# Kernel optimization log

Measured on AMD Instinct MI355X. Metric: run time of the kernel, lower is better.

Reference implementation:

```python
import jax, jax.numpy as jnp
import numpy as np

WIN = 12     # SAMv3 window_size
HEADS = 8    # num_heads

def _window(t, win=WIN):
    B, H, W, C = t.shape
    t = t.reshape(B, H // win, win, W // win, win, C).transpose(0, 1, 3, 2, 4, 5)
    return t.reshape(B, (H // win) * (W // win), win * win, C)

def _unwindow(t, H, W, win=WIN):
    B, nW, S, C = t.shape
    t = t.reshape(B, H // win, W // win, win, win, C).transpose(0, 1, 3, 2, 4, 5)
    return t.reshape(B, H, W, C)

def _sam(fq, fkv, bias, wq, wk, wv, wo, bo):
    # Windowed, masked cross-frame multi-head attention (SAMv3).
    # fq, fkv: (B, C, H, W); bias: (B, nW, 1, 1, S) additive mask bias.
    B, C, H, W = fq.shape
    hd = C // HEADS
    scale = hd ** -0.5
    q = _window(jnp.einsum('bchw,cd->bhwd', fq, wq))   # (B,nW,S,C)
    k = _window(jnp.einsum('bchw,cd->bhwd', fkv, wk))
    v = _window(jnp.einsum('bchw,cd->bhwd', fkv, wv))
    nW, S = q.shape[1], q.shape[2]
    q = q.reshape(B, nW, S, HEADS, hd)
    k = k.reshape(B, nW, S, HEADS, hd)
    v = v.reshape(B, nW, S, HEADS, hd)
    attn = jnp.einsum('bnqhd,bnkhd->bnhqk', q, k) * scale + bias
    attn = jax.nn.softmax(attn, axis=-1)
    out = jnp.einsum('bnhqk,bnkhd->bnqhd', attn, v).reshape(B, nW, S, C)
    out = out @ wo + bo
    return _unwindow(out, H, W).transpose(0, 3, 1, 2)  # (B, C, H, W)

def setup_inputs() -> dict:
    key = jax.random.key(0)
    B, C, T, H, W = 2, 384, 2, 192, 192
    ks = jax.random.split(key, 16)
    d = {}
    d['x'] = jax.random.normal(ks[0], (B, C, T, H, W), jnp.float32)
    d['mask'] = jax.random.randint(ks[1], (B, T, 1, H, W), 0, 2, jnp.int32)
    names = ['sam1_wq', 'sam1_wk', 'sam1_wv', 'sam1_wo',
             'sam2_wq', 'sam2_wk', 'sam2_wv', 'sam2_wo',
             'proj1_w', 'proj2_w']
    for i, n in enumerate(names):
        d[n] = jax.random.normal(ks[2 + i], (C, C), jnp.float32) * 0.02
    d['sam1_bo'] = jnp.zeros((C,), jnp.float32)
    d['sam2_bo'] = jnp.zeros((C,), jnp.float32)
    d['proj1_b'] = jnp.zeros((C,), jnp.float32)
    d['proj2_b'] = jnp.zeros((C,), jnp.float32)
    return d

def reference(x, mask, sam1_wq, sam1_wk, sam1_wv, sam1_wo, sam1_bo,
              sam2_wq, sam2_wk, sam2_wv, sam2_wo, sam2_bo,
              proj1_w, proj1_b, proj2_w, proj2_b):
    # x: (B, C, T=2, H, W); mask: (B, T, 1, H, W)
    f1 = x[:, :, 0]
    f2 = x[:, :, 1]
    m = mask[:, 1, 0][..., None]                      # (B, H, W, 1), frame-2 mask
    mw = _window(m)[..., 0]                           # (B, nW, S)
    bias = jnp.where(mw == 0, -1e9, 0.0).astype(x.dtype)[:, :, None, None, :]
    o1 = _sam(f1, f2, bias, sam1_wq, sam1_wk, sam1_wv, sam1_wo, sam1_bo)
    x1 = jnp.einsum('bchw,dc->bdhw', o1, proj1_w) + proj1_b[None, :, None, None]
    o2 = _sam(f2, f1, bias, sam2_wq, sam2_wk, sam2_wv, sam2_wo, sam2_bo)
    x2 = jnp.einsum('bchw,dc->bdhw', o2, proj2_w) + proj2_b[None, :, None, None]
    return jnp.concatenate([x1[:, :, None], x2[:, :, None]], axis=2)  # (B, C, 2, H, W)
```

## Files before the change

kernel.cpp:

```cpp
#include <hip/hip_runtime.h>
#include <stdint.h>

typedef __attribute__((ext_vector_type(8))) short bf16x8;
typedef __attribute__((ext_vector_type(4))) float f32x4;

#define HW    36864
#define CCH   384
#define NPIX  73728
#define W2    147456

__device__ __forceinline__ unsigned short f2bf(float f) {
  unsigned u = __builtin_bit_cast(unsigned, f);
  u += 0x7FFFu + ((u >> 16) & 1u);
  return (unsigned short)(u >> 16);
}

typedef const unsigned int __attribute__((address_space(1)))* gas1_t;
typedef unsigned int __attribute__((address_space(3)))* las3_t;
__device__ __forceinline__ void gload16(const void* g, void* l) {
  __builtin_amdgcn_global_load_lds((gas1_t)g, (las3_t)l, 16, 0, 0);
}


__global__ void k_wt(const float* __restrict__ w0, const float* __restrict__ w1,
                     const float* __restrict__ w2, const float* __restrict__ w3,
                     const float* __restrict__ w4, const float* __restrict__ w5,
                     unsigned short* __restrict__ wt) {
  int idx = blockIdx.x * 256 + threadIdx.x;
  int w = blockIdx.y;
  const float* W;
  switch (w) { case 0: W = w0; break; case 1: W = w1; break;
               case 2: W = w2; break; case 3: W = w3; break;
               case 4: W = w4; break; default: W = w5; break; }
  const int slotmap[6] = {0, 4, 5, 3, 1, 2};
  int slot = slotmap[w];
  int c = idx / 384, d = idx % 384;
  wt[(size_t)slot * W2 + (size_t)d * 384 + c] = f2bf(W[(size_t)c * 384 + d]);
}

__global__ void k_wf(const float* __restrict__ wo1, const float* __restrict__ pj1,
                     const float* __restrict__ wo2, const float* __restrict__ pj2,
                     unsigned short* __restrict__ wfT) {
  int idx = blockIdx.x * 256 + threadIdx.x;
  int s = blockIdx.y;
  const float* wo = s ? wo2 : wo1;
  const float* pj = s ? pj2 : pj1;
  int d = idx / 384, e = idx % 384;
  float acc = 0.f;
  for (int c = 0; c < 384; ++c) acc += pj[d * 384 + c] * wo[e * 384 + c];
  wfT[(size_t)s * W2 + (size_t)d * 384 + e] = f2bf(acc);
}

__global__ void k_bf(const float* __restrict__ bo1, const float* __restrict__ pj1,
                     const float* __restrict__ pb1, const float* __restrict__ bo2,
                     const float* __restrict__ pj2, const float* __restrict__ pb2,
                     float* __restrict__ bfused) {
  int t = threadIdx.x;
  int s = t / 384, d = t % 384;
  const float* bo = s ? bo2 : bo1;
  const float* pj = s ? pj2 : pj1;
  const float* pb = s ? pb2 : pb1;
  float acc = pb[d];
  for (int c = 0; c < 384; ++c) acc += pj[d * 384 + c] * bo[c];
  bfused[t] = acc;
}

__global__ __launch_bounds__(256) void k_tx(const float* __restrict__ x,
                                            unsigned short* __restrict__ xbf) {
  __shared__ float tile[64][65];
  int p0 = blockIdx.x * 64;
  int c0 = blockIdx.y * 64;
  int bt = blockIdx.z;
  int b = bt >> 1, t = bt & 1;
  int tid = threadIdx.x;
  int cl = tid >> 2;
  int pq = (tid & 3) * 4;
  const float* src = x + (((size_t)b * CCH + (c0 + cl)) * 2 + t) * HW + p0;
#pragma unroll
  for (int i = 0; i < 4; ++i) {
    int p_l = pq + i * 16;
    float4 v = *reinterpret_cast<const float4*>(src + p_l);
    tile[cl][p_l + 0] = v.x; tile[cl][p_l + 1] = v.y;
    tile[cl][p_l + 2] = v.z; tile[cl][p_l + 3] = v.w;
  }
  __syncthreads();
  int pl = tid >> 2;
  int cq = (tid & 3) * 16;
  unsigned short* dst = xbf + ((size_t)(t * 2 + b) * HW + p0 + pl) * CCH + c0 + cq;
  bf16x8 o0, o1;
#pragma unroll
  for (int j = 0; j < 8; ++j) o0[j] = (short)f2bf(tile[cq + j][pl]);
#pragma unroll
  for (int j = 0; j < 8; ++j) o1[j] = (short)f2bf(tile[cq + 8 + j][pl]);
  *reinterpret_cast<bf16x8*>(dst) = o0;
  *reinterpret_cast<bf16x8*>(dst + 8) = o1;
}

template <int EPI>
__global__ __launch_bounds__(256) void gemm_bt(
    const unsigned short* __restrict__ A,
    const unsigned short* __restrict__ Bt,
    unsigned short* __restrict__ Cq,
    unsigned short* __restrict__ Ckv,
    int nsplit,
    float* __restrict__ Cf,
    const float* __restrict__ bias,
    int tsel, float oscale) {
  __shared__ __align__(16) unsigned short Ash[2][4096];
  __shared__ __align__(16) unsigned short Bsh[2][4096];
  const int tid = threadIdx.x;
  const int lane = tid & 63;
  const int wid = tid >> 6, wr = wid >> 1, wc = wid & 1;

  const int gx = gridDim.x;
  const int nwg = gx * gridDim.y;
  const int bid = blockIdx.x + blockIdx.y * gx;
  const int chunk = nwg >> 3;
  const int l = (bid & 7) * chunk + (bid >> 3);
  const int bx = l % gx, by = l / gx;

  const int m0 = (EPI == 1 ? bx : by) * 128;
  const int n0 = (EPI == 1 ? by : bx) * 128;
  const int r15 = lane & 15, g = lane >> 4;

  const int u1 = tid + 256;
  const unsigned short* srcA0 = A + (size_t)(m0 + (tid >> 2)) * 384 + (((tid & 3) ^ ((tid >> 3) & 3)) << 3);
  const unsigned short* srcA1 = A + (size_t)(m0 + (u1 >> 2)) * 384 + (((u1 & 3) ^ ((u1 >> 3) & 3)) << 3);
  const unsigned short* srcB0 = Bt + (size_t)(n0 + (tid >> 2)) * 384 + (((tid & 3) ^ ((tid >> 3) & 3)) << 3);
  const unsigned short* srcB1 = Bt + (size_t)(n0 + (u1 >> 2)) * 384 + (((u1 & 3) ^ ((u1 >> 3) & 3)) << 3);
  const int wbase = (tid & ~63) * 8;

  f32x4 acc[4][4];
  f32x4 zero4 = {0.f, 0.f, 0.f, 0.f};
#pragma unroll
  for (int a = 0; a < 4; ++a)
#pragma unroll
    for (int b = 0; b < 4; ++b) acc[a][b] = zero4;

  const int swzr = (g ^ ((r15 >> 1) & 3)) << 3;

#define STAGE(cur, kt) do {                            \
    int ke = (kt) * 32;                                \
    gload16(srcA0 + ke, &Ash[(cur)][wbase]);           \
    gload16(srcA1 + ke, &Ash[(cur)][2048 + wbase]);    \
    gload16(srcB0 + ke, &Bsh[(cur)][wbase]);           \
    gload16(srcB1 + ke, &Bsh[(cur)][2048 + wbase]);    \
  } while (0)

  STAGE(0, 0);
  for (int kt = 0; kt < 12; ++kt) {
    const int cur = kt & 1;
    __syncthreads();
    if (kt < 11) STAGE(cur ^ 1, kt + 1);
    bf16x8 af[4], bfv[4];
#pragma unroll
    for (int a = 0; a < 4; ++a)
      af[a] = *(const bf16x8*)&Ash[cur][(wr * 64 + a * 16 + r15) * 32 + swzr];
#pragma unroll
    for (int b = 0; b < 4; ++b)
      bfv[b] = *(const bf16x8*)&Bsh[cur][(wc * 64 + b * 16 + r15) * 32 + swzr];
#pragma unroll
    for (int a = 0; a < 4; ++a)
#pragma unroll
      for (int b = 0; b < 4; ++b)
        acc[a][b] = __builtin_amdgcn_mfma_f32_16x16x32_bf16(af[a], bfv[b], acc[a][b], 0, 0, 0);
  }
#undef STAGE

  if (EPI == 2) {
    const int bb = m0 / HW;
    unsigned short* Cp;
    int ldc, nc0;
    float sc;
    if (n0 < nsplit) { Cp = Cq;  ldc = 384; nc0 = n0;          sc = oscale; }
    else             { Cp = Ckv; ldc = 768; nc0 = n0 - nsplit; sc = 1.0f;   }
#pragma unroll
    for (int a = 0; a < 4; ++a) {
#pragma unroll
      for (int r = 0; r < 4; ++r) {
        int m = m0 + wr * 64 + a * 16 + g * 4 + r;
        int p = m - bb * HW;
        int ph = p / 192, pw = p % 192;
        int wy = ph / 12, sy = ph % 12, wx = pw / 12, sx = pw % 12;
        size_t rowoff = ((size_t)bb * HW + (wy * 16 + wx) * 144 + sy * 12 + sx) * (size_t)ldc;
#pragma unroll
        for (int b = 0; b < 4; ++b) {
          int n = nc0 + wc * 64 + b * 16 + r15;
          Cp[rowoff + n] = f2bf(acc[a][b][r] * sc);
        }
      }
    }
  } else {
    int bb = n0 / HW;
#pragma unroll
    for (int a = 0; a < 4; ++a) {
      int d = m0 + wr * 64 + a * 16 + g * 4;
#pragma unroll
      for (int b = 0; b < 4; ++b) {
        int n = n0 + wc * 64 + b * 16 + r15;
        int p = n - bb * HW;
#pragma unroll
        for (int r = 0; r < 4; ++r) {
          float v = acc[a][b][r] + bias[d + r];
          Cf[(((size_t)bb * CCH + (d + r)) * 2 + tsel) * HW + p] = v;
        }
      }
    }
  }
}

__global__ __launch_bounds__(512, 2) void attn_kernel(
    const unsigned short* __restrict__ q,
    const unsigned short* __restrict__ kv,
    const int* __restrict__ mask,
    unsigned short* __restrict__ obuf) {
  __shared__ __align__(16) unsigned short P[8][16][168];
  const int n = blockIdx.x, b = blockIdx.y;
  const int tid = threadIdx.x;
  const int h = tid >> 6, lane = tid & 63;
  const int c15 = lane & 15, g = lane >> 4;
  const int wy = n >> 4, wx = n & 15;
  const unsigned short* qb = q  + ((size_t)b * HW + n * 144) * 384 + h * 48;
  const unsigned short* kb = kv + ((size_t)b * HW + n * 144) * 768 + h * 48;
  const unsigned short* vb = kb + 384;
  const int* mrow = mask + (size_t)(b * 2 + 1) * HW;

  for (int idx = lane; idx < 16 * 24; idx += 64)
    P[h][idx / 24][144 + (idx % 24)] = 0;

  float biasv[9];
#pragma unroll
  for (int nt = 0; nt < 9; ++nt) {
    int sk = nt * 16 + c15;
    int ph = wy * 12 + sk / 12, pw = wx * 12 + sk % 12;
    biasv[nt] = (mrow[ph * 192 + pw] == 0) ? -1e9f : 0.0f;
  }

  bf16x8 zfrag = {0, 0, 0, 0, 0, 0, 0, 0};
  f32x4 zero4 = {0.f, 0.f, 0.f, 0.f};

  bf16x8 kf0[9], kf1[9];
#pragma unroll
  for (int nt = 0; nt < 9; ++nt) {
    const unsigned short* kp = kb + (size_t)(nt * 16 + c15) * 768;
    kf0[nt] = *(const bf16x8*)(kp + g * 8);
    kf1[nt] = zfrag;
    if (g < 2) kf1[nt] = *(const bf16x8*)(kp + 32 + g * 8);
  }

  bf16x8 vf[5][3];
#pragma unroll
  for (int ks = 0; ks < 5; ++ks) {
#pragma unroll
    for (int dt = 0; dt < 3; ++dt) {
      bf16x8 v = {0, 0, 0, 0, 0, 0, 0, 0};
#pragma unroll
      for (int j = 0; j < 8; ++j) {
        int sk = ks * 32 + g * 8 + j;
        if (sk < 144)
          v[j] = (short)vb[(size_t)sk * 768 + dt * 16 + c15];
      }
      vf[ks][dt] = v;
    }
  }

  bf16x8 qf0, qf1;
  {
    const unsigned short* qp = qb + (size_t)c15 * 384;
    qf0 = *(const bf16x8*)(qp + g * 8);
    qf1 = zfrag;
    if (g < 2) qf1 = *(const bf16x8*)(qp + 32 + g * 8);
  }

  for (int mt = 0; mt < 9; ++mt) {
    bf16x8 qn0 = zfrag, qn1 = zfrag;
    if (mt < 8) {
      const unsigned short* qp = qb + (size_t)((mt + 1) * 16 + c15) * 384;
      qn0 = *(const bf16x8*)(qp + g * 8);
      if (g < 2) qn1 = *(const bf16x8*)(qp + 32 + g * 8);
    }

    float l4[4] = {0.f, 0.f, 0.f, 0.f};
    f32x4 oacc[3];
#pragma unroll
    for (int dt = 0; dt < 3; ++dt) oacc[dt] = zero4;

#pragma unroll
    for (int nt = 0; nt < 9; ++nt) {
      f32x4 s = __builtin_amdgcn_mfma_f32_16x16x32_bf16(qf1, kf1[nt], zero4, 0, 0, 0);
      s = __builtin_amdgcn_mfma_f32_16x16x32_bf16(qf0, kf0[nt], s, 0, 0, 0);
#pragma unroll
      for (int r = 0; r < 4; ++r) {
        float pv = __expf(s[r] + biasv[nt]);
        l4[r] += pv;
        P[h][g * 4 + r][nt * 16 + c15] = f2bf(pv);
      }
      if (nt & 1) {
        int ks = nt >> 1;
        bf16x8 pf = *(const bf16x8*)&P[h][c15][ks * 32 + g * 8];
#pragma unroll
        for (int dt = 0; dt < 3; ++dt)
          oacc[dt] = __builtin_amdgcn_mfma_f32_16x16x32_bf16(pf, vf[ks][dt], oacc[dt], 0, 0, 0);
      }
    }
    {
      bf16x8 pf = *(const bf16x8*)&P[h][c15][4 * 32 + g * 8];
#pragma unroll
      for (int dt = 0; dt < 3; ++dt)
        oacc[dt] = __builtin_amdgcn_mfma_f32_16x16x32_bf16(pf, vf[4][dt], oacc[dt], 0, 0, 0);
    }

#pragma unroll
    for (int s = 1; s < 16; s <<= 1)
#pragma unroll
      for (int r = 0; r < 4; ++r) l4[r] += __shfl_xor(l4[r], s, 64);

    float inv[4];
#pragma unroll
    for (int r = 0; r < 4; ++r) inv[r] = 1.0f / l4[r];
#pragma unroll
    for (int dt = 0; dt < 3; ++dt) {
#pragma unroll
      for (int r = 0; r < 4; ++r) {
        int so = mt * 16 + g * 4 + r;
        int oh = wy * 12 + so / 12, ow = wx * 12 + so % 12;
        obuf[((size_t)b * HW + oh * 192 + ow) * 384 + h * 48 + dt * 16 + c15] =
            f2bf(oacc[dt][r] * inv[r]);
      }
    }

    qf0 = qn0; qf1 = qn1;
  }
}

extern "C" void kernel_launch(void* const* d_in, const int* in_sizes, int n_in,
                              void* d_out, int out_size, void* d_ws, size_t ws_size,
                              hipStream_t stream) {
  const float* x    = (const float*)d_in[0];
  const int*   mask = (const int*)d_in[1];
  const float* wq1 = (const float*)d_in[2];
  const float* wk1 = (const float*)d_in[3];
  const float* wv1 = (const float*)d_in[4];
  const float* wo1 = (const float*)d_in[5];
  const float* wq2 = (const float*)d_in[6];
  const float* wk2 = (const float*)d_in[7];
  const float* wv2 = (const float*)d_in[8];
  const float* wo2 = (const float*)d_in[9];
  const float* pj1 = (const float*)d_in[10];
  const float* pj2 = (const float*)d_in[11];
  const float* bo1 = (const float*)d_in[12];
  const float* bo2 = (const float*)d_in[13];
  const float* pb1 = (const float*)d_in[14];
  const float* pb2 = (const float*)d_in[15];
  float* out = (float*)d_out;

  const float SCALE = 0.14433756729740643f;

  char* ws = (char*)d_ws;
  size_t off = 0;
  unsigned short* wt   = (unsigned short*)(ws + off); off += (size_t)6 * W2 * 2;
  unsigned short* wfT  = (unsigned short*)(ws + off); off += (size_t)2 * W2 * 2;
  float*          bfu  = (float*)(ws + off);          off += (size_t)2 * 384 * 4;
  unsigned short* xbf  = (unsigned short*)(ws + off); off += (size_t)4 * HW * CCH * 2;
  size_t fixed = off;

  size_t qsz = (size_t)NPIX * 384 * 2, kvsz = (size_t)NPIX * 768 * 2, osz = qsz;
  bool fused = (ws_size >= fixed + 2 * qsz + 2 * kvsz + osz);
  if (!fused && ws_size < fixed + qsz + kvsz + osz) return;

  k_wt<<<dim3(576, 6), 256, 0, stream>>>(wq1, wk1, wv1, wq2, wk2, wv2, wt);
  k_wf<<<dim3(576, 2), 256, 0, stream>>>(wo1, pj1, wo2, pj2, wfT);
  k_bf<<<1, 768, 0, stream>>>(bo1, pj1, pb1, bo2, pj2, pb2, bfu);
  k_tx<<<dim3(576, 6, 4), 256, 0, stream>>>(x, xbf);

  if (fused) {
    unsigned short* qb[2] = {(unsigned short*)(ws + fixed),
                             (unsigned short*)(ws + fixed + qsz)};
    unsigned short* kvb[2] = {(unsigned short*)(ws + fixed + 2 * qsz),
                              (unsigned short*)(ws + fixed + 2 * qsz + kvsz)};
    unsigned short* obuf = (unsigned short*)(ws + fixed + 2 * qsz + 2 * kvsz);
    for (int f = 0; f < 2; ++f) {
      gemm_bt<2><<<dim3(9, 576), 256, 0, stream>>>(
          xbf + (size_t)f * 2 * HW * CCH, wt + (size_t)f * 3 * W2,
          qb[f], kvb[1 - f], 384, nullptr, nullptr, 0, SCALE);
    }
    for (int s = 0; s < 2; ++s) {
      attn_kernel<<<dim3(256, 2), 512, 0, stream>>>(qb[s], kvb[s], mask, obuf);
      gemm_bt<1><<<dim3(3, 576), 256, 0, stream>>>(
          wfT + (size_t)s * W2, obuf, nullptr, nullptr, 0, out, bfu + s * 384, s, 1.0f);
    }
  } else {
    unsigned short* qbuf = (unsigned short*)(ws + fixed);
    unsigned short* kvbuf = (unsigned short*)(ws + fixed + qsz);
    unsigned short* obuf = (unsigned short*)(ws + fixed + qsz + kvsz);
    for (int s = 0; s < 2; ++s) {
      const unsigned short* fq = xbf + (size_t)(s == 0 ? 0 : 1) * 2 * HW * CCH;
      const unsigned short* fk = xbf + (size_t)(s == 0 ? 1 : 0) * 2 * HW * CCH;
      gemm_bt<2><<<dim3(3, 576), 256, 0, stream>>>(
          fq, wt + (size_t)(s == 0 ? 0 : 3) * W2, qbuf, nullptr, 384,
          nullptr, nullptr, 0, SCALE);
      gemm_bt<2><<<dim3(6, 576), 256, 0, stream>>>(
          fk, wt + (size_t)(s == 0 ? 4 : 1) * W2, nullptr, kvbuf, 0,
          nullptr, nullptr, 0, 1.0f);
      attn_kernel<<<dim3(256, 2), 512, 0, stream>>>(qbuf, kvbuf, mask, obuf);
      gemm_bt<1><<<dim3(3, 576), 256, 0, stream>>>(
          wfT + (size_t)s * W2, obuf, nullptr, nullptr, 0, out, bfu + s * 384, s, 1.0f);
    }
  }
}
```

Before: 723.6 us.

## Triple-buffer GEMM K-loop and move window gather into attention via pixel table

The GEMM mainloop moves from double to triple buffering in one combined LDS array. Prefetch now runs two stages ahead, and each step waits on a partial vmcnt plus a raw barrier instead of a full __syncthreads. The QKV GEMM epilogue no longer scatters rows into windowed order and writes plain row-major output. The attention kernel instead builds an LDS table of pixel offsets per window and gathers Q/K/V rows and scatters outputs through it. This aims to overlap global loads with MFMA and to cut the per-element index arithmetic in the epilogue, at the cost of more LDS per GEMM block and strided gathered loads in attention.

```diff
diff --git a/kernel.cpp b/kernel.cpp
--- a/kernel.cpp
+++ b/kernel.cpp
@@ -106,8 +106,7 @@
     float* __restrict__ Cf,
     const float* __restrict__ bias,
     int tsel, float oscale) {
-  __shared__ __align__(16) unsigned short Ash[2][4096];
-  __shared__ __align__(16) unsigned short Bsh[2][4096];
+  __shared__ __align__(16) unsigned short Lsh[3][8192];
   const int tid = threadIdx.x;
   const int lane = tid & 63;
   const int wid = tid >> 6, wr = wid >> 1, wc = wid & 1;
@@ -139,55 +138,59 @@
 
   const int swzr = (g ^ ((r15 >> 1) & 3)) << 3;
 
-#define STAGE(cur, kt) do {                            \
-    int ke = (kt) * 32;                                \
-    gload16(srcA0 + ke, &Ash[(cur)][wbase]);           \
-    gload16(srcA1 + ke, &Ash[(cur)][2048 + wbase]);    \
-    gload16(srcB0 + ke, &Bsh[(cur)][wbase]);           \
-    gload16(srcB1 + ke, &Bsh[(cur)][2048 + wbase]);    \
+#define STAGE(buf, kt) do {                                  \
+    int ke = (kt) * 32;                                      \
+    gload16(srcA0 + ke, &Lsh[(buf)][wbase]);                 \
+    gload16(srcA1 + ke, &Lsh[(buf)][2048 + wbase]);          \
+    gload16(srcB0 + ke, &Lsh[(buf)][4096 + wbase]);          \
+    gload16(srcB1 + ke, &Lsh[(buf)][6144 + wbase]);          \
   } while (0)
 
+#define COMPUTE(buf) do {                                                       \
+    bf16x8 af[4], bfv[4];                                                       \
+    _Pragma("unroll")                                                           \
+    for (int a = 0; a < 4; ++a)                                                 \
+      af[a] = *(const bf16x8*)&Lsh[(buf)][(wr * 64 + a * 16 + r15) * 32 + swzr];\
+    _Pragma("unroll")                                                           \
+    for (int b = 0; b < 4; ++b)                                                 \
+      bfv[b] = *(const bf16x8*)&Lsh[(buf)][4096 + (wc * 64 + b * 16 + r15) * 32 + swzr];\
+    _Pragma("unroll")                                                           \
+    for (int a = 0; a < 4; ++a)                                                 \
+      _Pragma("unroll")                                                         \
+      for (int b = 0; b < 4; ++b)                                               \
+        acc[a][b] = __builtin_amdgcn_mfma_f32_16x16x32_bf16(af[a], bfv[b], acc[a][b], 0, 0, 0);\
+  } while (0)
+
   STAGE(0, 0);
-  for (int kt = 0; kt < 12; ++kt) {
-    const int cur = kt & 1;
-    __syncthreads();
-    if (kt < 11) STAGE(cur ^ 1, kt + 1);
-    bf16x8 af[4], bfv[4];
-#pragma unroll
-    for (int a = 0; a < 4; ++a)
-      af[a] = *(const bf16x8*)&Ash[cur][(wr * 64 + a * 16 + r15) * 32 + swzr];
-#pragma unroll
-    for (int b = 0; b < 4; ++b)
-      bfv[b] = *(const bf16x8*)&Bsh[cur][(wc * 64 + b * 16 + r15) * 32 + swzr];
-#pragma unroll
-    for (int a = 0; a < 4; ++a)
-#pragma unroll
-      for (int b = 0; b < 4; ++b)
-        acc[a][b] = __builtin_amdgcn_mfma_f32_16x16x32_bf16(af[a], bfv[b], acc[a][b], 0, 0, 0);
-  }
+  STAGE(1, 1);
+#pragma unroll
+  for (int kt = 0; kt < 11; ++kt) {
+    asm volatile("s_waitcnt vmcnt(4)" ::: "memory");
+    __builtin_amdgcn_s_barrier();
+    asm volatile("" ::: "memory");
+    if (kt < 10) STAGE((kt + 2) % 3, kt + 2);
+    COMPUTE(kt % 3);
+  }
+  __syncthreads();
+  COMPUTE(11 % 3);
 #undef STAGE
+#undef COMPUTE
 
   if (EPI == 2) {
-    const int bb = m0 / HW;
     unsigned short* Cp;
-    int ldc, nc0;
+    int ldc2, ncol0;
     float sc;
-    if (n0 < nsplit) { Cp = Cq;  ldc = 384; nc0 = n0;          sc = oscale; }
-    else             { Cp = Ckv; ldc = 768; nc0 = n0 - nsplit; sc = 1.0f;   }
+    if (n0 < nsplit) { Cp = Cq;  ldc2 = 384; ncol0 = n0;          sc = oscale; }
+    else             { Cp = Ckv; ldc2 = 768; ncol0 = n0 - nsplit; sc = 1.0f;   }
 #pragma unroll
     for (int a = 0; a < 4; ++a) {
-#pragma unroll
-      for (int r = 0; r < 4; ++r) {
-        int m = m0 + wr * 64 + a * 16 + g * 4 + r;
-        int p = m - bb * HW;
-        int ph = p / 192, pw = p % 192;
-        int wy = ph / 12, sy = ph % 12, wx = pw / 12, sx = pw % 12;
-        size_t rowoff = ((size_t)bb * HW + (wy * 16 + wx) * 144 + sy * 12 + sx) * (size_t)ldc;
-#pragma unroll
-        for (int b = 0; b < 4; ++b) {
-          int n = nc0 + wc * 64 + b * 16 + r15;
-          Cp[rowoff + n] = f2bf(acc[a][b][r] * sc);
-        }
+      size_t rbase = (size_t)(m0 + wr * 64 + a * 16 + g * 4) * ldc2;
+#pragma unroll
+      for (int b = 0; b < 4; ++b) {
+        int n = ncol0 + wc * 64 + b * 16 + r15;
+        unsigned short* cp = Cp + rbase + n;
+#pragma unroll
+        for (int r = 0; r < 4; ++r) cp[(size_t)r * ldc2] = f2bf(acc[a][b][r] * sc);
       }
     }
   } else {
@@ -215,26 +218,26 @@
     const int* __restrict__ mask,
     unsigned short* __restrict__ obuf) {
   __shared__ __align__(16) unsigned short P[8][16][168];
+  __shared__ int ptab[144];
   const int n = blockIdx.x, b = blockIdx.y;
   const int tid = threadIdx.x;
   const int h = tid >> 6, lane = tid & 63;
   const int c15 = lane & 15, g = lane >> 4;
   const int wy = n >> 4, wx = n & 15;
-  const unsigned short* qb = q  + ((size_t)b * HW + n * 144) * 384 + h * 48;
-  const unsigned short* kb = kv + ((size_t)b * HW + n * 144) * 768 + h * 48;
-  const unsigned short* vb = kb + 384;
+  const size_t rowbase = (size_t)b * HW;
   const int* mrow = mask + (size_t)(b * 2 + 1) * HW;
+
+  if (tid < 144)
+    ptab[tid] = (wy * 12 + tid / 12) * 192 + wx * 12 + tid % 12;
 
   for (int idx = lane; idx < 16 * 24; idx += 64)
     P[h][idx / 24][144 + (idx % 24)] = 0;
+  __syncthreads();
 
   float biasv[9];
 #pragma unroll
-  for (int nt = 0; nt < 9; ++nt) {
-    int sk = nt * 16 + c15;
-    int ph = wy * 12 + sk / 12, pw = wx * 12 + sk % 12;
-    biasv[nt] = (mrow[ph * 192 + pw] == 0) ? -1e9f : 0.0f;
-  }
+  for (int nt = 0; nt < 9; ++nt)
+    biasv[nt] = (mrow[ptab[nt * 16 + c15]] == 0) ? -1e9f : 0.0f;
 
   bf16x8 zfrag = {0, 0, 0, 0, 0, 0, 0, 0};
   f32x4 zero4 = {0.f, 0.f, 0.f, 0.f};
@@ -242,12 +245,13 @@
   bf16x8 kf0[9], kf1[9];
 #pragma unroll
   for (int nt = 0; nt < 9; ++nt) {
-    const unsigned short* kp = kb + (size_t)(nt * 16 + c15) * 768;
+    const unsigned short* kp = kv + (rowbase + ptab[nt * 16 + c15]) * 768 + h * 48;
     kf0[nt] = *(const bf16x8*)(kp + g * 8);
     kf1[nt] = zfrag;
     if (g < 2) kf1[nt] = *(const bf16x8*)(kp + 32 + g * 8);
   }
 
+  const unsigned short* vb = kv + rowbase * 768 + 384 + h * 48;
   bf16x8 vf[5][3];
 #pragma unroll
   for (int ks = 0; ks < 5; ++ks) {
@@ -258,7 +262,7 @@
       for (int j = 0; j < 8; ++j) {
         int sk = ks * 32 + g * 8 + j;
         if (sk < 144)
-          v[j] = (short)vb[(size_t)sk * 768 + dt * 16 + c15];
+          v[j] = (short)vb[(size_t)ptab[sk] * 768 + dt * 16 + c15];
       }
       vf[ks][dt] = v;
     }
@@ -266,7 +270,7 @@
 
   bf16x8 qf0, qf1;
   {
-    const unsigned short* qp = qb + (size_t)c15 * 384;
+    const unsigned short* qp = q + (rowbase + ptab[c15]) * 384 + h * 48;
     qf0 = *(const bf16x8*)(qp + g * 8);
     qf1 = zfrag;
     if (g < 2) qf1 = *(const bf16x8*)(qp + 32 + g * 8);
@@ -275,7 +279,7 @@
   for (int mt = 0; mt < 9; ++mt) {
     bf16x8 qn0 = zfrag, qn1 = zfrag;
     if (mt < 8) {
-      const unsigned short* qp = qb + (size_t)((mt + 1) * 16 + c15) * 384;
+      const unsigned short* qp = q + (rowbase + ptab[(mt + 1) * 16 + c15]) * 384 + h * 48;
       qn0 = *(const bf16x8*)(qp + g * 8);
       if (g < 2) qn1 = *(const bf16x8*)(qp + 32 + g * 8);
     }
@@ -323,8 +327,7 @@
 #pragma unroll
       for (int r = 0; r < 4; ++r) {
         int so = mt * 16 + g * 4 + r;
-        int oh = wy * 12 + so / 12, ow = wx * 12 + so % 12;
-        obuf[((size_t)b * HW + oh * 192 + ow) * 384 + h * 48 + dt * 16 + c15] =
+        obuf[(rowbase + ptab[so]) * 384 + h * 48 + dt * 16 + c15] =
             f2bf(oacc[dt][r] * inv[r]);
       }
     }
```

Measured after the change: 678.4 us, median of 4. 6.3% less time.
